# Performance work log

Measured on AMD Instinct MI355X. Metric: run time of the kernel, lower is better.

Reference implementation:

```python
import jax, jax.numpy as jnp
import numpy as np

IN_DIM, BANDS = 42, 22
H_VAD, H_NOISE, H_DEN = 24, 48, 96


def gru(x, w_ih, w_hh, b_ih, b_hh):
    """torch.nn.GRU (batch_first) semantics, h0=0.
    x: [B,T,D]; w_ih: [3H,D]; w_hh: [3H,H]; gate order r,z,n."""
    H = w_hh.shape[1]
    # precompute input projections for all timesteps (big GEMM, recurrence only on H)
    xp = jnp.einsum('btd,gd->btg', x, w_ih) + b_ih  # [B,T,3H]

    def step(h, xt):
        hp = h @ w_hh.T + b_hh
        xr, xz, xn = jnp.split(xt, 3, axis=-1)
        hr, hz, hn = jnp.split(hp, 3, axis=-1)
        r = jax.nn.sigmoid(xr + hr)
        z = jax.nn.sigmoid(xz + hz)
        n = jnp.tanh(xn + r * hn)
        h_new = (1.0 - z) * n + z * h
        return h_new, h_new

    h0 = jnp.zeros((x.shape[0], H), x.dtype)
    _, hs = jax.lax.scan(step, h0, jnp.swapaxes(xp, 0, 1))  # [T,B,H]
    return jnp.swapaxes(hs, 0, 1)  # [B,T,H]


def setup_inputs() -> dict:
    key = jax.random.key(0)
    ks = jax.random.split(key, 20)

    def w(k, shape, fan):
        return (jax.random.normal(k, shape, jnp.float32) / np.sqrt(fan)).astype(jnp.float32)

    B, T = 256, 2000
    d_noise_in = H_VAD + H_VAD + IN_DIM     # 90
    d_den_in = H_VAD + H_NOISE + IN_DIM     # 114
    return {
        'x': jax.random.normal(ks[0], (B, T, IN_DIM), jnp.float32),
        'in_w': w(ks[1], (H_VAD, IN_DIM), IN_DIM),
        'in_b': jnp.zeros((H_VAD,), jnp.float32),
        'vad_wih': w(ks[2], (3 * H_VAD, H_VAD), H_VAD),
        'vad_whh': w(ks[3], (3 * H_VAD, H_VAD), H_VAD),
        'vad_bih': jnp.zeros((3 * H_VAD,), jnp.float32),
        'vad_bhh': jnp.zeros((3 * H_VAD,), jnp.float32),
        'vad_out_w': w(ks[4], (1, H_VAD), H_VAD),
        'vad_out_b': jnp.zeros((1,), jnp.float32),
        'noise_wih': w(ks[5], (3 * H_NOISE, d_noise_in), d_noise_in),
        'noise_whh': w(ks[6], (3 * H_NOISE, H_NOISE), H_NOISE),
        'noise_bih': jnp.zeros((3 * H_NOISE,), jnp.float32),
        'noise_bhh': jnp.zeros((3 * H_NOISE,), jnp.float32),
        'den_wih': w(ks[7], (3 * H_DEN, d_den_in), d_den_in),
        'den_whh': w(ks[8], (3 * H_DEN, H_DEN), H_DEN),
        'den_bih': jnp.zeros((3 * H_DEN,), jnp.float32),
        'den_bhh': jnp.zeros((3 * H_DEN,), jnp.float32),
        'out_w': w(ks[9], (BANDS, H_DEN), H_DEN),
        'out_b': jnp.zeros((BANDS,), jnp.float32),
    }


def reference(x, in_w, in_b, vad_wih, vad_whh, vad_bih, vad_bhh,
              vad_out_w, vad_out_b, noise_wih, noise_whh, noise_bih, noise_bhh,
              den_wih, den_whh, den_bih, den_bhh, out_w, out_b):
    tmp = jnp.tanh(jnp.einsum('btd,hd->bth', x, in_w) + in_b)          # [B,T,24]
    vad_h = gru(tmp, vad_wih, vad_whh, vad_bih, vad_bhh)               # [B,T,24]
    vad = jax.nn.sigmoid(jnp.einsum('bth,oh->bto', vad_h, vad_out_w) + vad_out_b)
    noise_in = jnp.concatenate([tmp, vad_h, x], axis=-1)               # [B,T,90]
    noise_h = gru(noise_in, noise_wih, noise_whh, noise_bih, noise_bhh)  # [B,T,48]
    den_in = jnp.concatenate([vad_h, noise_h, x], axis=-1)             # [B,T,114]
    den_h = gru(den_in, den_wih, den_whh, den_bih, den_bhh)            # [B,T,96]
    gains = jax.nn.sigmoid(jnp.einsum('bth,oh->bto', den_h, out_w) + out_b)
    return gains, vad
```

## Files before the change

### kernel.cpp

```cpp
#include <hip/hip_runtime.h>

typedef _Float16 f16;
typedef _Float16 h2 __attribute__((ext_vector_type(2)));
typedef unsigned int u32;

#define TB  256
#define TTT 2000
#define INW 42
#define HV  24
#define HN  48
#define HD  96
#define NTH 640

#define DIN 0
#define DH  128
#define NIN 224
#define NH  320
#define ACTW 384

__device__ __forceinline__ float fsigm(float v) {
    return __builtin_amdgcn_rcpf(1.0f + __builtin_amdgcn_exp2f(-1.44269504089f * v));
}
__device__ __forceinline__ float ftanh(float v) {
    float e = __builtin_amdgcn_exp2f(2.88539008178f * v);
    return 1.0f - 2.0f * __builtin_amdgcn_rcpf(e + 1.0f);
}
__device__ __forceinline__ float dot2f(u32 a, u32 w, float c) {
#if __has_builtin(__builtin_amdgcn_fdot2)
    return __builtin_amdgcn_fdot2(__builtin_bit_cast(h2, a), __builtin_bit_cast(h2, w), c, false);
#else
    h2 av = __builtin_bit_cast(h2, a), wv = __builtin_bit_cast(h2, w);
    return c + (float)av[0] * (float)wv[0] + (float)av[1] * (float)wv[1];
#endif
}
__device__ __forceinline__ u32 packw(float a, float b) {
    h2 v; v[0] = (f16)a; v[1] = (f16)b;
    return __builtin_bit_cast(u32, v);
}
template<int CTRL>
__device__ __forceinline__ float dpp_add(float x) {
    int y = __builtin_amdgcn_mov_dpp(__builtin_bit_cast(int, x), CTRL, 0xF, 0xF, true);
    return x + __builtin_bit_cast(float, y);
}

#define SYNCB() asm volatile("s_waitcnt lgkmcnt(0)\n\ts_barrier" ::: "memory")

#define ACCI(AV, W, IDX) do { u32 _a = (AV); \
    rr = dot2f(_a, W[0][IDX], rr); zz = dot2f(_a, W[1][IDX], zz); an = dot2f(_a, W[2][IDX], an); } while (0)
#define ACCH(AV, W, IDX) do { u32 _a = (AV); \
    rr = dot2f(_a, W[0][IDX], rr); zz = dot2f(_a, W[1][IDX], zz); hn = dot2f(_a, W[2][IDX], hn); } while (0)
#define ACCI4(U4, W, M0) do { uint4 _u4 = (U4); \
    ACCI(_u4.x, W, (M0)+0); ACCI(_u4.y, W, (M0)+1); ACCI(_u4.z, W, (M0)+2); ACCI(_u4.w, W, (M0)+3); } while (0)
#define ACCH4(U4, W, M0) do { uint4 _u4 = (U4); \
    ACCH(_u4.x, W, (M0)+0); ACCH(_u4.y, W, (M0)+1); ACCH(_u4.z, W, (M0)+2); ACCH(_u4.w, W, (M0)+3); } while (0)
#define RED4_Q() do { \
    rr = dpp_add<0xB1>(rr); rr = dpp_add<0x4E>(rr); \
    zz = dpp_add<0xB1>(zz); zz = dpp_add<0x4E>(zz); \
    an = dpp_add<0xB1>(an); an = dpp_add<0x4E>(an); \
    hn = dpp_add<0xB1>(hn); hn = dpp_add<0x4E>(hn); } while (0)
#define RED4_1() do { \
    rr = dpp_add<0xB1>(rr); zz = dpp_add<0xB1>(zz); \
    an = dpp_add<0xB1>(an); hn = dpp_add<0xB1>(hn); } while (0)

template<int N> struct IC { static constexpr int val = N; };

__global__ __launch_bounds__(NTH, 2) void rnnoise_kernel(
    const float* __restrict__ gx,
    const float* __restrict__ in_w,      const float* __restrict__ in_b,
    const float* __restrict__ vad_wih,   const float* __restrict__ vad_whh,
    const float* __restrict__ vad_bih,   const float* __restrict__ vad_bhh,
    const float* __restrict__ vad_out_w, const float* __restrict__ vad_out_b,
    const float* __restrict__ noise_wih, const float* __restrict__ noise_whh,
    const float* __restrict__ noise_bih, const float* __restrict__ noise_bhh,
    const float* __restrict__ den_wih,   const float* __restrict__ den_whh,
    const float* __restrict__ den_bih,   const float* __restrict__ den_bhh,
    const float* __restrict__ out_w,     const float* __restrict__ out_b,
    float* __restrict__ gains, float* __restrict__ vout)
{
    __shared__ __align__(16) f16 act[4][ACTW];

    const int tid = threadIdx.x, wid = tid >> 6, lane = tid & 63;
    const int b = blockIdx.x;

    if (tid < 768) ((u32*)act)[tid] = 0u;
    if (tid + NTH < 768) ((u32*)act)[tid + NTH] = 0u;
    __syncthreads();

    const int role = (wid == 9) ? 2 : ((wid == 4 || wid == 5 || wid == 8) ? 1 : 0);

    if (role == 0) {
        const int dwi = (wid < 4) ? wid : (wid - 2);
        const int u = 16 * dwi + (lane >> 2), q = lane & 3;
        u32 wdi[3][16], wdh[3][12];
        #pragma unroll
        for (int g = 0; g < 3; ++g) {
            const float* wi = den_wih + (g * HD + u) * 114;
            #pragma unroll
            for (int m = 0; m < 16; ++m) {
                int c = 32 * q + 2 * m;
                float a  = (c     < 114) ? wi[c]     : 0.f;
                float b2 = (c + 1 < 114) ? wi[c + 1] : 0.f;
                wdi[g][m] = packw(a, b2);
            }
            const float* wh = den_whh + (g * HD + u) * HD + 24 * q;
            #pragma unroll
            for (int m = 0; m < 12; ++m) wdh[g][m] = packw(wh[2*m], wh[2*m+1]);
        }
        const float bdr  = den_bih[u]        + den_bhh[u];
        const float bdz  = den_bih[HD + u]   + den_bhh[HD + u];
        const float bdni = den_bih[2*HD + u];
        const float bdnh = den_bhh[2*HD + u];
        float hreg = 0.f;

        auto step = [&](auto PC, int k) {
            constexpr int P  = decltype(PC)::val;
            constexpr int SI = (P + 1) & 3;
            if (k >= 3 && k <= TTT + 2) {
                float rr = 0, zz = 0, an = 0, hn = 0;
                const uint4* hp = (const uint4*)&act[P][DH + 24 * q];
                uint4 h0 = hp[0], h1 = hp[1], h2 = hp[2];
                const uint4* ip = (const uint4*)&act[SI][DIN + 32 * q];
                uint4 a0 = ip[0], a1 = ip[1], a2 = ip[2], a3 = ip[3];
                ACCI4(a0, wdi, 0); ACCI4(a1, wdi, 4); ACCI4(a2, wdi, 8); ACCI4(a3, wdi, 12);
                ACCH4(h0, wdh, 0); ACCH4(h1, wdh, 4); ACCH4(h2, wdh, 8);
                RED4_Q();
                if (q == 0) {
                    float r = fsigm(rr + bdr);
                    float z = fsigm(zz + bdz);
                    float n = ftanh(an + bdni + r * (hn + bdnh));
                    hreg = z * (hreg - n) + n;
                    act[SI][DH + u] = (f16)hreg;
                }
            }
            SYNCB();
        };
        #pragma clang loop unroll(disable)
        for (int k0 = 0; k0 < TTT + 4; k0 += 4) {
            step(IC<0>{}, k0); step(IC<1>{}, k0+1); step(IC<2>{}, k0+2); step(IC<3>{}, k0+3);
        }

    } else if (role == 1) {
        const int nwi = (wid == 4) ? 0 : ((wid == 5) ? 1 : 2);
        const int u = 16 * nwi + (lane >> 2), q = lane & 3;
        const int o = 8 * nwi + (lane >> 3), s8 = lane & 7;
        const int oc = (o < 22) ? o : 0;
        u32 wni[3][12], wnh[3][8], wo[6];
        #pragma unroll
        for (int g = 0; g < 3; ++g) {
            const float* wi = noise_wih + (g * HN + u) * 90;
            #pragma unroll
            for (int m = 0; m < 12; ++m) {
                int c = 24 * q + 2 * m;
                float a  = (c     < 90) ? wi[c]     : 0.f;
                float b2 = (c + 1 < 90) ? wi[c + 1] : 0.f;
                wni[g][m] = packw(a, b2);
            }
            const float* wh = noise_whh + (g * HN + u) * HN;
            #pragma unroll
            for (int m = 0; m < 8; ++m) {
                int c = 16 * q + 2 * m;
                float a  = (c     < 48) ? wh[c]     : 0.f;
                float b2 = (c + 1 < 48) ? wh[c + 1] : 0.f;
                wnh[g][m] = packw(a, b2);
            }
        }
        #pragma unroll
        for (int m = 0; m < 6; ++m)
            wo[m] = packw(out_w[oc*HD + 12*s8 + 2*m], out_w[oc*HD + 12*s8 + 2*m + 1]);
        const float bnr  = noise_bih[u]        + noise_bhh[u];
        const float bnz  = noise_bih[HN + u]   + noise_bhh[HN + u];
        const float bnni = noise_bih[2*HN + u];
        const float bnnh = noise_bhh[2*HN + u];
        const float bo   = out_b[oc];
        float hreg = 0.f;

        auto step = [&](auto PC, int k) {
            constexpr int P   = decltype(PC)::val;
            constexpr int SI  = (P + 2) & 3;
            constexpr int SH  = (P + 1) & 3;
            if (k >= 2 && k <= TTT + 1) {
                float rr = 0, zz = 0, an = 0, hn = 0;
                const uint4* hp = (const uint4*)&act[SH][NH + 16 * q];
                uint4 h0 = hp[0], h1 = hp[1];
                const uint4* ip = (const uint4*)&act[SI][NIN + 24 * q];
                uint4 a0 = ip[0], a1 = ip[1], a2 = ip[2];
                ACCI4(a0, wni, 0); ACCI4(a1, wni, 4); ACCI4(a2, wni, 8);
                ACCH4(h0, wnh, 0); ACCH4(h1, wnh, 4);
                RED4_Q();
                if (q == 0) {
                    float r = fsigm(rr + bnr);
                    float z = fsigm(zz + bnz);
                    float n = ftanh(an + bnni + r * (hn + bnnh));
                    hreg = z * (hreg - n) + n;
                    f16 hh = (f16)hreg;
                    act[SI][NH + u]       = hh;
                    act[SI][DIN + 24 + u] = hh;
                }
            }
            if (k >= 4) {
                float acc = 0;
                const uint2* dp = (const uint2*)&act[P][DH + 12 * s8];
                uint2 d0 = dp[0], d1 = dp[1], d2 = dp[2];
                acc = dot2f(d0.x, wo[0], acc); acc = dot2f(d0.y, wo[1], acc);
                acc = dot2f(d1.x, wo[2], acc); acc = dot2f(d1.y, wo[3], acc);
                acc = dot2f(d2.x, wo[4], acc); acc = dot2f(d2.y, wo[5], acc);
                acc = dpp_add<0xB1>(acc); acc = dpp_add<0x4E>(acc);
                acc += __shfl_xor(acc, 4);
                if (s8 == 0 && o < 22)
                    gains[((size_t)b * TTT + (k - 4)) * 22 + o] = fsigm(acc + bo);
            }
            SYNCB();
        };
        #pragma clang loop unroll(disable)
        for (int k0 = 0; k0 < TTT + 4; k0 += 4) {
            step(IC<0>{}, k0); step(IC<1>{}, k0+1); step(IC<2>{}, k0+2); step(IC<3>{}, k0+3);
        }

    } else {
        const int l = lane;
        const int u = (l < 48) ? (l >> 1) : 0, q2 = l & 1;
        u32 wvi[3][6], wvh[3][6], wtm[12];
        float bvr = 0, bvz = 0, bvni = 0, bvnh = 0, btm = 0, wvo_u = 0;
        if (l < 48) {
            #pragma unroll
            for (int g = 0; g < 3; ++g) {
                const float* wi = vad_wih + (g * HV + u) * HV + 12 * q2;
                const float* wh = vad_whh + (g * HV + u) * HV + 12 * q2;
                #pragma unroll
                for (int j = 0; j < 6; ++j) {
                    wvi[g][j] = packw(wi[2*j], wi[2*j+1]);
                    wvh[g][j] = packw(wh[2*j], wh[2*j+1]);
                }
            }
            #pragma unroll
            for (int j = 0; j < 12; ++j) {
                int c0 = 24 * q2 + 2 * j;
                float a = (c0     < INW) ? in_w[u * INW + c0]     : 0.f;
                float c = (c0 + 1 < INW) ? in_w[u * INW + c0 + 1] : 0.f;
                wtm[j] = packw(a, c);
            }
            bvr  = vad_bih[u]        + vad_bhh[u];
            bvz  = vad_bih[HV + u]   + vad_bhh[HV + u];
            bvni = vad_bih[2*HV + u];
            bvnh = vad_bhh[2*HV + u];
            btm  = in_b[u];
            if (q2 == 0) wvo_u = vad_out_w[u];
        }
        const float bvo = vad_out_b[0];
        float hreg = 0.f;

        float xa = 0, xb = 0, xc = 0, xd = 0;
        if (l < INW) {
            xa = gx[((size_t)b * TTT + 0) * INW + l];
            xb = gx[((size_t)b * TTT + 1) * INW + l];
            xc = gx[((size_t)b * TTT + 2) * INW + l];
            xd = gx[((size_t)b * TTT + 3) * INW + l];
        }

        auto step = [&](auto PC, int k) {
            constexpr int P  = decltype(PC)::val;
            constexpr int ST = (P + 3) & 3;
            constexpr int SH = (P + 2) & 3;
            if (k < TTT && l < INW) {
                float xv;
                if constexpr (P == 0) xv = xa; else if constexpr (P == 1) xv = xb;
                else if constexpr (P == 2) xv = xc; else xv = xd;
                f16 xh = (f16)xv;
                act[P][NIN + 48 + l] = xh;
                act[P][DIN + 72 + l] = xh;
            }
            if (k + 4 < TTT && l < INW) {
                float xv = gx[((size_t)b * TTT + (k + 4)) * INW + l];
                if constexpr (P == 0) xa = xv; else if constexpr (P == 1) xb = xv;
                else if constexpr (P == 2) xc = xv; else xd = xv;
            }
            if (k >= 1 && k <= TTT) {
                float rr = 0, zz = 0, an = 0, hn = 0;
                if (l < 48) {
                    const uint2* tp = (const uint2*)&act[ST][NIN + 12 * q2];
                    const uint2* hp = (const uint2*)&act[SH][NIN + 24 + 12 * q2];
                    #pragma unroll
                    for (int v = 0; v < 3; ++v) {
                        uint2 a = tp[v]; ACCI(a.x, wvi, 2*v); ACCI(a.y, wvi, 2*v+1);
                        uint2 h = hp[v]; ACCH(h.x, wvh, 2*v); ACCH(h.y, wvh, 2*v+1);
                    }
                    RED4_1();
                    if (q2 == 0) {
                        float r = fsigm(rr + bvr);
                        float z = fsigm(zz + bvz);
                        float n = ftanh(an + bvni + r * (hn + bvnh));
                        hreg = z * (hreg - n) + n;
                        f16 hh = (f16)hreg;
                        act[ST][NIN + 24 + u] = hh;
                        act[ST][DIN + u]      = hh;
                    }
                }
                float val = (l < 48 && q2 == 0) ? (wvo_u * hreg) : 0.f;
                val = dpp_add<0xB1>(val);  val = dpp_add<0x4E>(val);
                val = dpp_add<0x124>(val); val = dpp_add<0x128>(val);
                val += __shfl_xor(val, 16); val += __shfl_xor(val, 32);
                if (l == 0) vout[(size_t)b * TTT + (k - 1)] = fsigm(val + bvo);
            }
            if (k < TTT && l < 48) {
                float acc = 0;
                const uint4* xp = (const uint4*)&act[P][NIN + 48 + 24 * q2];
                uint4 a = xp[0], b2 = xp[1], c2 = xp[2];
                acc = dot2f(a.x,  wtm[0], acc);  acc = dot2f(a.y,  wtm[1], acc);
                acc = dot2f(a.z,  wtm[2], acc);  acc = dot2f(a.w,  wtm[3], acc);
                acc = dot2f(b2.x, wtm[4], acc);  acc = dot2f(b2.y, wtm[5], acc);
                acc = dot2f(b2.z, wtm[6], acc);  acc = dot2f(b2.w, wtm[7], acc);
                acc = dot2f(c2.x, wtm[8], acc);  acc = dot2f(c2.y, wtm[9], acc);
                acc = dot2f(c2.z, wtm[10], acc); acc = dot2f(c2.w, wtm[11], acc);
                acc = dpp_add<0xB1>(acc);
                if (q2 == 0) act[P][NIN + u] = (f16)ftanh(acc + btm);
            }
            SYNCB();
        };
        #pragma clang loop unroll(disable)
        for (int k0 = 0; k0 < TTT + 4; k0 += 4) {
            step(IC<0>{}, k0); step(IC<1>{}, k0+1); step(IC<2>{}, k0+2); step(IC<3>{}, k0+3);
        }
    }
}

extern "C" void kernel_launch(void* const* d_in, const int* in_sizes, int n_in,
                              void* d_out, int out_size, void* d_ws, size_t ws_size,
                              hipStream_t stream) {
    (void)in_sizes; (void)n_in; (void)d_ws; (void)ws_size; (void)out_size;
    const float* gx        = (const float*)d_in[0];
    const float* in_w      = (const float*)d_in[1];
    const float* in_b      = (const float*)d_in[2];
    const float* vad_wih   = (const float*)d_in[3];
    const float* vad_whh   = (const float*)d_in[4];
    const float* vad_bih   = (const float*)d_in[5];
    const float* vad_bhh   = (const float*)d_in[6];
    const float* vad_out_w = (const float*)d_in[7];
    const float* vad_out_b = (const float*)d_in[8];
    const float* noise_wih = (const float*)d_in[9];
    const float* noise_whh = (const float*)d_in[10];
    const float* noise_bih = (const float*)d_in[11];
    const float* noise_bhh = (const float*)d_in[12];
    const float* den_wih   = (const float*)d_in[13];
    const float* den_whh   = (const float*)d_in[14];
    const float* den_bih   = (const float*)d_in[15];
    const float* den_bhh   = (const float*)d_in[16];
    const float* out_w     = (const float*)d_in[17];
    const float* out_b     = (const float*)d_in[18];
    float* gains = (float*)d_out;
    float* vout  = (float*)d_out + (size_t)TB * (size_t)TTT * 22;

    rnnoise_kernel<<<dim3(TB), dim3(NTH), 0, stream>>>(
        gx, in_w, in_b, vad_wih, vad_whh, vad_bih, vad_bhh, vad_out_w, vad_out_b,
        noise_wih, noise_whh, noise_bih, noise_bhh, den_wih, den_whh, den_bih, den_bhh,
        out_w, out_b, gains, vout);
}
```

Before: 1.893 ms.

## Deepen activation ring to 8 slots and precompute GRU input projections one step ahead

Expands the shared-memory activation ring from 4 to 8 time slots and reschedules the den and noise GRU stages. The input-projection dot products for the next timestep are computed after the hidden-state update and carried in registers, so only the recurrent matvec stays on the critical path of each barrier step. The gain output projection is moved to a later slot. The launch-bounds occupancy hint is dropped from 2 to 1 block per CU, which gives more register room but allows less block-level overlap.

```diff
diff --git a/kernel.cpp b/kernel.cpp
--- a/kernel.cpp
+++ b/kernel.cpp
@@ -64,7 +64,7 @@
 
 template<int N> struct IC { static constexpr int val = N; };
 
-__global__ __launch_bounds__(NTH, 2) void rnnoise_kernel(
+__global__ __launch_bounds__(NTH, 1) void rnnoise_kernel(
     const float* __restrict__ gx,
     const float* __restrict__ in_w,      const float* __restrict__ in_b,
     const float* __restrict__ vad_wih,   const float* __restrict__ vad_whh,
@@ -77,13 +77,16 @@
     const float* __restrict__ out_w,     const float* __restrict__ out_b,
     float* __restrict__ gains, float* __restrict__ vout)
 {
-    __shared__ __align__(16) f16 act[4][ACTW];
+    __shared__ __align__(16) f16 act[8][ACTW];
 
     const int tid = threadIdx.x, wid = tid >> 6, lane = tid & 63;
     const int b = blockIdx.x;
 
-    if (tid < 768) ((u32*)act)[tid] = 0u;
-    if (tid + NTH < 768) ((u32*)act)[tid + NTH] = 0u;
+    #pragma unroll
+    for (int i = 0; i < 3; ++i) {
+        int idx = tid + i * NTH;
+        if (idx < 8 * ACTW / 2) ((u32*)act)[idx] = 0u;
+    }
     __syncthreads();
 
     const int role = (wid == 9) ? 2 : ((wid == 4 || wid == 5 || wid == 8) ? 1 : 0);
@@ -111,17 +114,22 @@
         const float bdni = den_bih[2*HD + u];
         const float bdnh = den_bhh[2*HD + u];
         float hreg = 0.f;
+        float rr = 0.f, zz = 0.f, an = 0.f;
 
         auto step = [&](auto PC, int k) {
-            constexpr int P  = decltype(PC)::val;
-            constexpr int SI = (P + 1) & 3;
-            if (k >= 3 && k <= TTT + 2) {
-                float rr = 0, zz = 0, an = 0, hn = 0;
-                const uint4* hp = (const uint4*)&act[P][DH + 24 * q];
+            constexpr int P   = decltype(PC)::val;
+            constexpr int SHH = (P + 2) & 7;
+            constexpr int SWR = (P + 3) & 7;
+            constexpr int SB  = (P + 4) & 7;
+            uint4 a0{}, a1{}, a2{}, a3{};
+            if (k >= 4 && k < TTT + 4) {
+                const uint4* ip = (const uint4*)&act[SB][DIN + 32 * q];
+                a0 = ip[0]; a1 = ip[1]; a2 = ip[2]; a3 = ip[3];
+            }
+            if (k >= 5 && k < TTT + 5) {
+                const uint4* hp = (const uint4*)&act[SHH][DH + 24 * q];
                 uint4 h0 = hp[0], h1 = hp[1], h2 = hp[2];
-                const uint4* ip = (const uint4*)&act[SI][DIN + 32 * q];
-                uint4 a0 = ip[0], a1 = ip[1], a2 = ip[2], a3 = ip[3];
-                ACCI4(a0, wdi, 0); ACCI4(a1, wdi, 4); ACCI4(a2, wdi, 8); ACCI4(a3, wdi, 12);
+                float hn = 0.f;
                 ACCH4(h0, wdh, 0); ACCH4(h1, wdh, 4); ACCH4(h2, wdh, 8);
                 RED4_Q();
                 if (q == 0) {
@@ -129,14 +137,19 @@
                     float z = fsigm(zz + bdz);
                     float n = ftanh(an + bdni + r * (hn + bdnh));
                     hreg = z * (hreg - n) + n;
-                    act[SI][DH + u] = (f16)hreg;
+                    act[SWR][DH + u] = (f16)hreg;
                 }
+                rr = 0.f; zz = 0.f; an = 0.f;
+            }
+            if (k >= 4 && k < TTT + 4) {
+                ACCI4(a0, wdi, 0); ACCI4(a1, wdi, 4); ACCI4(a2, wdi, 8); ACCI4(a3, wdi, 12);
             }
             SYNCB();
         };
         #pragma clang loop unroll(disable)
-        for (int k0 = 0; k0 < TTT + 4; k0 += 4) {
-            step(IC<0>{}, k0); step(IC<1>{}, k0+1); step(IC<2>{}, k0+2); step(IC<3>{}, k0+3);
+        for (int k0 = 0; k0 < TTT + 8; k0 += 8) {
+            step(IC<0>{},k0);   step(IC<1>{},k0+1); step(IC<2>{},k0+2); step(IC<3>{},k0+3);
+            step(IC<4>{},k0+4); step(IC<5>{},k0+5); step(IC<6>{},k0+6); step(IC<7>{},k0+7);
         }
 
     } else if (role == 1) {
@@ -173,18 +186,28 @@
         const float bnnh = noise_bhh[2*HN + u];
         const float bo   = out_b[oc];
         float hreg = 0.f;
+        float rr = 0.f, zz = 0.f, an = 0.f;
 
         auto step = [&](auto PC, int k) {
             constexpr int P   = decltype(PC)::val;
-            constexpr int SI  = (P + 2) & 3;
-            constexpr int SH  = (P + 1) & 3;
-            if (k >= 2 && k <= TTT + 1) {
-                float rr = 0, zz = 0, an = 0, hn = 0;
-                const uint4* hp = (const uint4*)&act[SH][NH + 16 * q];
+            constexpr int SHH = (P + 4) & 7;
+            constexpr int SWR = (P + 5) & 7;
+            constexpr int SB  = (P + 6) & 7;
+            constexpr int SOT = (P + 2) & 7;
+            uint4 a0{}, a1{}, a2{};
+            if (k >= 2 && k < TTT + 2) {
+                const uint4* ip = (const uint4*)&act[SB][NIN + 24 * q];
+                a0 = ip[0]; a1 = ip[1]; a2 = ip[2];
+            }
+            uint2 d0{}, d1{}, d2{};
+            if (k >= 6 && k < TTT + 6) {
+                const uint2* dp = (const uint2*)&act[SOT][DH + 12 * s8];
+                d0 = dp[0]; d1 = dp[1]; d2 = dp[2];
+            }
+            if (k >= 3 && k < TTT + 3) {
+                const uint4* hp = (const uint4*)&act[SHH][NH + 16 * q];
                 uint4 h0 = hp[0], h1 = hp[1];
-                const uint4* ip = (const uint4*)&act[SI][NIN + 24 * q];
-                uint4 a0 = ip[0], a1 = ip[1], a2 = ip[2];
-                ACCI4(a0, wni, 0); ACCI4(a1, wni, 4); ACCI4(a2, wni, 8);
+                float hn = 0.f;
                 ACCH4(h0, wnh, 0); ACCH4(h1, wnh, 4);
                 RED4_Q();
                 if (q == 0) {
@@ -193,27 +216,30 @@
                     float n = ftanh(an + bnni + r * (hn + bnnh));
                     hreg = z * (hreg - n) + n;
                     f16 hh = (f16)hreg;
-                    act[SI][NH + u]       = hh;
-                    act[SI][DIN + 24 + u] = hh;
+                    act[SWR][NH + u]       = hh;
+                    act[SWR][DIN + 24 + u] = hh;
                 }
-            }
-            if (k >= 4) {
+                rr = 0.f; zz = 0.f; an = 0.f;
+            }
+            if (k >= 6 && k < TTT + 6) {
                 float acc = 0;
-                const uint2* dp = (const uint2*)&act[P][DH + 12 * s8];
-                uint2 d0 = dp[0], d1 = dp[1], d2 = dp[2];
                 acc = dot2f(d0.x, wo[0], acc); acc = dot2f(d0.y, wo[1], acc);
                 acc = dot2f(d1.x, wo[2], acc); acc = dot2f(d1.y, wo[3], acc);
                 acc = dot2f(d2.x, wo[4], acc); acc = dot2f(d2.y, wo[5], acc);
                 acc = dpp_add<0xB1>(acc); acc = dpp_add<0x4E>(acc);
                 acc += __shfl_xor(acc, 4);
                 if (s8 == 0 && o < 22)
-                    gains[((size_t)b * TTT + (k - 4)) * 22 + o] = fsigm(acc + bo);
+                    gains[((size_t)b * TTT + (k - 6)) * 22 + o] = fsigm(acc + bo);
+            }
+            if (k >= 2 && k < TTT + 2) {
+                ACCI4(a0, wni, 0); ACCI4(a1, wni, 4); ACCI4(a2, wni, 8);
             }
             SYNCB();
         };
         #pragma clang loop unroll(disable)
-        for (int k0 = 0; k0 < TTT + 4; k0 += 4) {
-            step(IC<0>{}, k0); step(IC<1>{}, k0+1); step(IC<2>{}, k0+2); step(IC<3>{}, k0+3);
+        for (int k0 = 0; k0 < TTT + 8; k0 += 8) {
+            step(IC<0>{},k0);   step(IC<1>{},k0+1); step(IC<2>{},k0+2); step(IC<3>{},k0+3);
+            step(IC<4>{},k0+4); step(IC<5>{},k0+5); step(IC<6>{},k0+6); step(IC<7>{},k0+7);
         }
 
     } else {
@@ -259,20 +285,20 @@
 
         auto step = [&](auto PC, int k) {
             constexpr int P  = decltype(PC)::val;
-            constexpr int ST = (P + 3) & 3;
-            constexpr int SH = (P + 2) & 3;
+            constexpr int ST = (P + 7) & 7;
+            constexpr int SH = (P + 6) & 7;
             if (k < TTT && l < INW) {
                 float xv;
-                if constexpr (P == 0) xv = xa; else if constexpr (P == 1) xv = xb;
-                else if constexpr (P == 2) xv = xc; else xv = xd;
+                if constexpr ((P & 3) == 0) xv = xa; else if constexpr ((P & 3) == 1) xv = xb;
+                else if constexpr ((P & 3) == 2) xv = xc; else xv = xd;
                 f16 xh = (f16)xv;
                 act[P][NIN + 48 + l] = xh;
                 act[P][DIN + 72 + l] = xh;
             }
             if (k + 4 < TTT && l < INW) {
                 float xv = gx[((size_t)b * TTT + (k + 4)) * INW + l];
-                if constexpr (P == 0) xa = xv; else if constexpr (P == 1) xb = xv;
-                else if constexpr (P == 2) xc = xv; else xd = xv;
+                if constexpr ((P & 3) == 0) xa = xv; else if constexpr ((P & 3) == 1) xb = xv;
+                else if constexpr ((P & 3) == 2) xc = xv; else xd = xv;
             }
             if (k >= 1 && k <= TTT) {
                 float rr = 0, zz = 0, an = 0, hn = 0;
@@ -317,8 +343,9 @@
             SYNCB();
         };
         #pragma clang loop unroll(disable)
-        for (int k0 = 0; k0 < TTT + 4; k0 += 4) {
-            step(IC<0>{}, k0); step(IC<1>{}, k0+1); step(IC<2>{}, k0+2); step(IC<3>{}, k0+3);
+        for (int k0 = 0; k0 < TTT + 8; k0 += 8) {
+            step(IC<0>{},k0);   step(IC<1>{},k0+1); step(IC<2>{},k0+2); step(IC<3>{},k0+3);
+            step(IC<4>{},k0+4); step(IC<5>{},k0+5); step(IC<6>{},k0+6); step(IC<7>{},k0+7);
         }
     }
 }
```

Result: slower. 1.959 ms (+3.5%).
